# Performance work log

Measured on AMD Instinct MI355X. Metric: run time of the kernel, lower is better.

## Reference

```python
import jax, jax.numpy as jnp
import numpy as np

NUM_EXPERTS = 8
TOP_K = 2
HIDDEN = 1024
INTER = 4096
STD = 0.02


def setup_inputs() -> dict:
    key = jax.random.key(0)
    k0, k1, k2, k3 = jax.random.split(key, 4)
    hidden_states = jax.random.normal(k0, (2, 2048, HIDDEN), dtype=jnp.float32)
    gate_w = jax.random.normal(k1, (NUM_EXPERTS, HIDDEN), dtype=jnp.float32) * (HIDDEN ** -0.5)
    w1 = jax.random.normal(k2, (NUM_EXPERTS, INTER, HIDDEN), dtype=jnp.float32) * STD  # c_fc.weight
    w2 = jax.random.normal(k3, (NUM_EXPERTS, HIDDEN, INTER), dtype=jnp.float32) * STD  # c_proj.weight
    return {"hidden_states": hidden_states, "gate_w": gate_w, "w1": w1, "w2": w2}


def reference(hidden_states, gate_w, w1, w2):
    B, S, H = hidden_states.shape
    x = hidden_states.reshape(-1, H)                      # [T, H]
    T = x.shape[0]
    # ---- routing ----
    router_logits = x @ gate_w.T                          # [T, E]
    top_vals, top_idx = jax.lax.top_k(router_logits, TOP_K)
    router_weights = jax.nn.softmax(top_vals.astype(jnp.float32), axis=-1).astype(x.dtype)
    # dense combine matrix with exactly top_k nonzeros per row (math-equivalent
    # to the sort/grouped-GEMM/scatter-combine pipeline in the torch module)
    combine = jnp.zeros((T, NUM_EXPERTS), x.dtype).at[
        jnp.arange(T)[:, None], top_idx
    ].set(router_weights)                                 # [T, E]
    # ---- experts ----
    h = jax.nn.gelu(jnp.einsum('th,eih->eti', x, w1), approximate=False)  # [E, T, I]
    y = jnp.einsum('eti,ehi->eth', h, w2)                 # [E, T, H]
    out = jnp.einsum('eth,te->th', y, combine)            # weighted combine
    return out.reshape(B, S, H), router_logits
```

## Files before the change

### kernel.cpp

```cpp
#include <hip/hip_runtime.h>

#define T 4096
#define Hdim 1024
#define Idim 4096
#define NE 8
#define OUT0 4194304
#define SPLITK 2
#define BK 64

#define SLOT_CAP 9216

#define W1B_OFF 0u
#define W2B_OFF 67108864u
#define XB_OFF  134217728u
#define HB_OFF  142606336u
#define YB_OFF  218103808u
#define META_OFF 255852544u
#define M_COUNTS 0
#define M_CURS   8
#define M_OFFS   16
#define M_TEXP   32
#define M_TSLOT  8224
#define M_STOK   16416
#define M_TWF    25632

typedef short bf16x8 __attribute__((ext_vector_type(8)));
typedef float f32x4  __attribute__((ext_vector_type(4)));

__device__ __forceinline__ unsigned short f2bf(float f) {
    unsigned int b = __float_as_uint(f);
    b += 0x7fffu + ((b >> 16) & 1u);
    return (unsigned short)(b >> 16);
}
__device__ __forceinline__ float bf2f(unsigned short s) {
    return __uint_as_float(((unsigned int)s) << 16);
}

__device__ __forceinline__ void gl_lds16(const void* g, void* l) {
    __builtin_amdgcn_global_load_lds((const __attribute__((address_space(1))) void*)g,
                                     (__attribute__((address_space(3))) void*)l,
                                     16, 0, 0);
}

__global__ void zero_k(int* meta) {
    int i = blockIdx.x * blockDim.x + threadIdx.x;
    if (i < 16) meta[i] = 0;
    if (i < SLOT_CAP) meta[M_STOK + i] = -1;
}

__global__ void cvt_w_k(const float* __restrict__ w1, const float* __restrict__ w2,
                        unsigned short* __restrict__ w1b, unsigned short* __restrict__ w2b,
                        int n4each) {
    int i = blockIdx.x * blockDim.x + threadIdx.x;
    const float4* src; ushort4* dst; int j;
    if (i < n4each) { src = (const float4*)w1; dst = (ushort4*)w1b; j = i; }
    else            { src = (const float4*)w2; dst = (ushort4*)w2b; j = i - n4each; }
    float4 v = src[j];
    ushort4 o;
    o.x = f2bf(v.x); o.y = f2bf(v.y); o.z = f2bf(v.z); o.w = f2bf(v.w);
    dst[j] = o;
}

__global__ void router_k(const float* __restrict__ x, const float* __restrict__ gw,
                         float* __restrict__ logits_out, int* __restrict__ texp,
                         float* __restrict__ twf, int* __restrict__ counts,
                         unsigned short* __restrict__ xb) {
    int wv = threadIdx.x >> 6, lane = threadIdx.x & 63;
    int t = blockIdx.x * 4 + wv;
    const float* xp = x + (size_t)t * Hdim;
    unsigned short* xbp = xb + (size_t)t * Hdim;
    float s[NE];
    #pragma unroll
    for (int e = 0; e < NE; e++) s[e] = 0.f;
    #pragma unroll
    for (int j = 0; j < 16; j++) {
        float xv = xp[lane + 64 * j];
        xbp[lane + 64 * j] = f2bf(xv);
        #pragma unroll
        for (int e = 0; e < NE; e++) s[e] += xv * gw[e * Hdim + lane + 64 * j];
    }
    #pragma unroll
    for (int e = 0; e < NE; e++) {
        #pragma unroll
        for (int off = 32; off > 0; off >>= 1) s[e] += __shfl_xor(s[e], off);
    }
    if (lane == 0) {
        #pragma unroll
        for (int e = 0; e < NE; e++) logits_out[t * NE + e] = s[e];
        int i0 = 0; float v0 = s[0];
        #pragma unroll
        for (int e = 1; e < NE; e++) if (s[e] > v0) { v0 = s[e]; i0 = e; }
        int i1 = -1; float v1 = -3.4e38f;
        #pragma unroll
        for (int e = 0; e < NE; e++) if (e != i0 && s[e] > v1) { v1 = s[e]; i1 = e; }
        float e1 = expf(v1 - v0);
        float inv = 1.f / (1.f + e1);
        texp[2 * t] = i0; texp[2 * t + 1] = i1;
        twf[2 * t] = inv; twf[2 * t + 1] = e1 * inv;
        atomicAdd(&counts[i0], 1);
        atomicAdd(&counts[i1], 1);
    }
}

__global__ void offsets_k(const int* __restrict__ counts, int* __restrict__ offs) {
    if (threadIdx.x == 0 && blockIdx.x == 0) {
        int a = 0; offs[0] = 0;
        for (int e = 0; e < NE; e++) { a += (counts[e] + 127) & ~127; offs[e + 1] = a; }
    }
}

__global__ void assign_k(const int* __restrict__ texp, const int* __restrict__ offs,
                         int* __restrict__ curs, int* __restrict__ stok, int* __restrict__ tslot) {
    int p = blockIdx.x * blockDim.x + threadIdx.x;
    int e = texp[p];
    int slot = offs[e] + atomicAdd(&curs[e], 1);
    stok[slot] = p >> 1;
    tslot[p] = slot;
}

__global__ __launch_bounds__(256) void gemm1_k(
    const unsigned short* __restrict__ xb, const unsigned short* __restrict__ w1b,
    const int* __restrict__ offs, const int* __restrict__ stok,
    unsigned short* __restrict__ hb) {
    __shared__ __align__(16) unsigned short As[128 * BK];
    __shared__ __align__(16) unsigned short Bs[128 * BK];
    const int rt = blockIdx.y, ct = blockIdx.x;
    const int row0 = rt * 128;
    if (row0 >= offs[NE]) return;
    int e = 0;
    #pragma unroll
    for (int q = 1; q < NE; q++) if (offs[q] <= row0) e = q;

    const int tid = threadIdx.x;
    const int lane = tid & 63, wv = tid >> 6;
    const int srow = lane >> 3;
    const int schunk = (lane & 7) ^ srow;

    const unsigned short* gA[4]; const unsigned short* gB[4];
    unsigned short *lA[4], *lB[4];
    #pragma unroll
    for (int i = 0; i < 4; i++) {
        int r = wv * 32 + i * 8 + srow;
        int t = stok[row0 + r]; if (t < 0) t = 0;
        gA[i] = xb + (size_t)t * Hdim + schunk * 8;
        gB[i] = w1b + ((size_t)e * Idim + ct * 128 + r) * Hdim + schunk * 8;
        lA[i] = As + (wv * 32 + i * 8) * BK;
        lB[i] = Bs + (wv * 32 + i * 8) * BK;
    }

    f32x4 acc[4][4] = {};
    const int mrow = (wv & 1) * 64, ncol = (wv >> 1) * 64;
    const int fr = lane & 15, qd = lane >> 4;

    for (int kk = 0; kk < Hdim; kk += BK) {
        #pragma unroll
        for (int i = 0; i < 4; i++) {
            gl_lds16(gA[i] + kk, lA[i]);
            gl_lds16(gB[i] + kk, lB[i]);
        }
        __syncthreads();
        #pragma unroll
        for (int ko = 0; ko < 2; ko++) {
            bf16x8 af[4], bff[4];
            #pragma unroll
            for (int mi = 0; mi < 4; mi++)
                af[mi]  = *(const bf16x8*)&As[(mrow + mi * 16 + fr) * BK + ((((ko << 2) | qd) ^ (fr & 7)) << 3)];
            #pragma unroll
            for (int ni = 0; ni < 4; ni++)
                bff[ni] = *(const bf16x8*)&Bs[(ncol + ni * 16 + fr) * BK + ((((ko << 2) | qd) ^ (fr & 7)) << 3)];
            #pragma unroll
            for (int mi = 0; mi < 4; mi++)
                #pragma unroll
                for (int ni = 0; ni < 4; ni++)
                    acc[mi][ni] = __builtin_amdgcn_mfma_f32_16x16x32_bf16(af[mi], bff[ni], acc[mi][ni], 0, 0, 0);
        }
        __syncthreads();
    }
    #pragma unroll
    for (int mi = 0; mi < 4; mi++) {
        #pragma unroll
        for (int ni = 0; ni < 4; ni++) {
            #pragma unroll
            for (int r = 0; r < 4; r++) {
                int row = row0 + mrow + mi * 16 + qd * 4 + r;
                int col = ct * 128 + ncol + ni * 16 + fr;
                float v = acc[mi][ni][r];
                float u = v * (1.f + 0.044715f * v * v);
                float g = v / (1.f + __expf(-1.5957691216f * u));
                hb[(size_t)row * Idim + col] = f2bf(g);
            }
        }
    }
}

__global__ __launch_bounds__(256) void gemm2_k(
    const unsigned short* __restrict__ hb, const unsigned short* __restrict__ w2b,
    const int* __restrict__ offs, unsigned short* __restrict__ y16) {
    __shared__ __align__(16) unsigned short As[128 * BK];
    __shared__ __align__(16) unsigned short Bs[128 * BK];
    const int id = blockIdx.x;
    const int k8 = id & 7;
    const int j  = id >> 3;
    const int ct = j & 7;
    const int j8 = j >> 3;
    const int rtL = j8 % 9, kz = j8 / 9;
    const int rt = k8 * 9 + rtL;
    const int row0 = rt * 128;
    if (row0 >= offs[NE]) return;
    int e = 0;
    #pragma unroll
    for (int q = 1; q < NE; q++) if (offs[q] <= row0) e = q;

    const int tid = threadIdx.x;
    const int lane = tid & 63, wv = tid >> 6;
    const int srow = lane >> 3;
    const int schunk = (lane & 7) ^ srow;

    const unsigned short* gA[4]; const unsigned short* gB[4];
    unsigned short *lA[4], *lB[4];
    #pragma unroll
    for (int i = 0; i < 4; i++) {
        int r = wv * 32 + i * 8 + srow;
        gA[i] = hb + (size_t)(row0 + r) * Idim + schunk * 8;
        gB[i] = w2b + ((size_t)e * Hdim + ct * 128 + r) * Idim + schunk * 8;
        lA[i] = As + (wv * 32 + i * 8) * BK;
        lB[i] = Bs + (wv * 32 + i * 8) * BK;
    }

    f32x4 acc[4][4] = {};
    const int mrow = (wv & 1) * 64, ncol = (wv >> 1) * 64;
    const int fr = lane & 15, qd = lane >> 4;

    const int k0 = kz * (Idim / SPLITK), k1 = k0 + (Idim / SPLITK);
    for (int kk = k0; kk < k1; kk += BK) {
        #pragma unroll
        for (int i = 0; i < 4; i++) {
            gl_lds16(gA[i] + kk, lA[i]);
            gl_lds16(gB[i] + kk, lB[i]);
        }
        __syncthreads();
        #pragma unroll
        for (int ko = 0; ko < 2; ko++) {
            bf16x8 af[4], bff[4];
            #pragma unroll
            for (int mi = 0; mi < 4; mi++)
                af[mi]  = *(const bf16x8*)&As[(mrow + mi * 16 + fr) * BK + ((((ko << 2) | qd) ^ (fr & 7)) << 3)];
            #pragma unroll
            for (int ni = 0; ni < 4; ni++)
                bff[ni] = *(const bf16x8*)&Bs[(ncol + ni * 16 + fr) * BK + ((((ko << 2) | qd) ^ (fr & 7)) << 3)];
            #pragma unroll
            for (int mi = 0; mi < 4; mi++)
                #pragma unroll
                for (int ni = 0; ni < 4; ni++)
                    acc[mi][ni] = __builtin_amdgcn_mfma_f32_16x16x32_bf16(af[mi], bff[ni], acc[mi][ni], 0, 0, 0);
        }
        __syncthreads();
    }
    unsigned short* yk = y16 + (size_t)kz * SLOT_CAP * Hdim;
    #pragma unroll
    for (int mi = 0; mi < 4; mi++) {
        #pragma unroll
        for (int ni = 0; ni < 4; ni++) {
            #pragma unroll
            for (int r = 0; r < 4; r++) {
                int row = row0 + mrow + mi * 16 + qd * 4 + r;
                int col = ct * 128 + ncol + ni * 16 + fr;
                yk[(size_t)row * Hdim + col] = f2bf(acc[mi][ni][r]);
            }
        }
    }
}

__global__ void combine_k(const unsigned short* __restrict__ y16, const int* __restrict__ tslot,
                          const float* __restrict__ twf, float* __restrict__ out) {
    int i = blockIdx.x * blockDim.x + threadIdx.x;
    int t = i >> 7, rem = i & 127;
    int s0 = tslot[2 * t], s1 = tslot[2 * t + 1];
    float w0 = twf[2 * t], w1 = twf[2 * t + 1];
    const uint4* y0 = (const uint4*)(y16);
    const uint4* y1 = (const uint4*)(y16 + (size_t)SLOT_CAP * Hdim);
    uint4 a0 = y0[(size_t)s0 * 128 + rem];
    uint4 a1 = y1[(size_t)s0 * 128 + rem];
    uint4 b0 = y0[(size_t)s1 * 128 + rem];
    uint4 b1 = y1[(size_t)s1 * 128 + rem];
    float o[8];
    #pragma unroll
    for (int j = 0; j < 4; j++) {
        unsigned int ua0 = ((const unsigned int*)&a0)[j], ua1 = ((const unsigned int*)&a1)[j];
        unsigned int ub0 = ((const unsigned int*)&b0)[j], ub1 = ((const unsigned int*)&b1)[j];
        float alo = bf2f((unsigned short)ua0) + bf2f((unsigned short)ua1);
        float ahi = bf2f((unsigned short)(ua0 >> 16)) + bf2f((unsigned short)(ua1 >> 16));
        float blo = bf2f((unsigned short)ub0) + bf2f((unsigned short)ub1);
        float bhi = bf2f((unsigned short)(ub0 >> 16)) + bf2f((unsigned short)(ub1 >> 16));
        o[2 * j]     = w0 * alo + w1 * blo;
        o[2 * j + 1] = w0 * ahi + w1 * bhi;
    }
    float4* out4 = (float4*)out;
    out4[2 * i]     = make_float4(o[0], o[1], o[2], o[3]);
    out4[2 * i + 1] = make_float4(o[4], o[5], o[6], o[7]);
}

extern "C" void kernel_launch(void* const* d_in, const int* in_sizes, int n_in,
                              void* d_out, int out_size, void* d_ws, size_t ws_size,
                              hipStream_t stream) {
    const float* x  = (const float*)d_in[0];
    const float* gw = (const float*)d_in[1];
    const float* w1 = (const float*)d_in[2];
    const float* w2 = (const float*)d_in[3];
    float* out = (float*)d_out;

    char* ws = (char*)d_ws;
    unsigned short* w1b = (unsigned short*)(ws + W1B_OFF);
    unsigned short* w2b = (unsigned short*)(ws + W2B_OFF);
    unsigned short* xb  = (unsigned short*)(ws + XB_OFF);
    unsigned short* hb  = (unsigned short*)(ws + HB_OFF);
    unsigned short* y16 = (unsigned short*)(ws + YB_OFF);
    int*            meta = (int*)(ws + META_OFF);
    int* counts = meta + M_COUNTS;
    int* curs   = meta + M_CURS;
    int* offs   = meta + M_OFFS;
    int* texp   = meta + M_TEXP;
    int* tslot  = meta + M_TSLOT;
    int* stok   = meta + M_STOK;
    float* twf  = (float*)(meta + M_TWF);

    zero_k<<<36, 256, 0, stream>>>(meta);
    cvt_w_k<<<65536, 256, 0, stream>>>(w1, w2, w1b, w2b, NE * Idim * Hdim / 4);
    router_k<<<T / 4, 256, 0, stream>>>(x, gw, out + OUT0, texp, twf, counts, xb);
    offsets_k<<<1, 64, 0, stream>>>(counts, offs);
    assign_k<<<32, 256, 0, stream>>>(texp, offs, curs, stok, tslot);
    gemm1_k<<<dim3(Idim / 128, SLOT_CAP / 128), 256, 0, stream>>>(xb, w1b, offs, stok, hb);
    gemm2_k<<<(Hdim / 128) * (SLOT_CAP / 128) * SPLITK, 256, 0, stream>>>(hb, w2b, offs, y16);
    combine_k<<<T * Hdim / 8 / 256, 256, 0, stream>>>(y16, tslot, twf, out);
}
```

Baseline: 672.3 us.

## Register-prefetch next K tile in expert GEMMs instead of direct global-to-LDS loads

Replaces the direct global_load_lds async copies in both expert GEMM kernels with register-staged prefetch. The next K-slice is loaded into registers while MFMAs run on the current LDS tile, then written to LDS between two barriers. This aims to hide global load latency behind compute, which the previous load-then-sync loop could not do. The cost is extra VGPRs, which may lower occupancy, plus an additional barrier per iteration.

```diff
diff --git a/kernel.cpp b/kernel.cpp
--- a/kernel.cpp
+++ b/kernel.cpp
@@ -36,12 +36,6 @@
     return __uint_as_float(((unsigned int)s) << 16);
 }
 
-__device__ __forceinline__ void gl_lds16(const void* g, void* l) {
-    __builtin_amdgcn_global_load_lds((const __attribute__((address_space(1))) void*)g,
-                                     (__attribute__((address_space(3))) void*)l,
-                                     16, 0, 0);
-}
-
 __global__ void zero_k(int* meta) {
     int i = blockIdx.x * blockDim.x + threadIdx.x;
     if (i < 16) meta[i] = 0;
@@ -137,28 +131,38 @@
     const int schunk = (lane & 7) ^ srow;
 
     const unsigned short* gA[4]; const unsigned short* gB[4];
-    unsigned short *lA[4], *lB[4];
+    unsigned short *lds_a[4], *lds_b[4];
     #pragma unroll
     for (int i = 0; i < 4; i++) {
         int r = wv * 32 + i * 8 + srow;
         int t = stok[row0 + r]; if (t < 0) t = 0;
         gA[i] = xb + (size_t)t * Hdim + schunk * 8;
         gB[i] = w1b + ((size_t)e * Idim + ct * 128 + r) * Hdim + schunk * 8;
-        lA[i] = As + (wv * 32 + i * 8) * BK;
-        lB[i] = Bs + (wv * 32 + i * 8) * BK;
+        lds_a[i] = As + (wv * 32 + i * 8) * BK + lane * 8;
+        lds_b[i] = Bs + (wv * 32 + i * 8) * BK + lane * 8;
     }
 
     f32x4 acc[4][4] = {};
     const int mrow = (wv & 1) * 64, ncol = (wv >> 1) * 64;
     const int fr = lane & 15, qd = lane >> 4;
 
-    for (int kk = 0; kk < Hdim; kk += BK) {
-        #pragma unroll
-        for (int i = 0; i < 4; i++) {
-            gl_lds16(gA[i] + kk, lA[i]);
-            gl_lds16(gB[i] + kk, lB[i]);
-        }
-        __syncthreads();
+    uint4 ra[4], rb[4];
+    #pragma unroll
+    for (int i = 0; i < 4; i++) { ra[i] = *(const uint4*)(gA[i]); rb[i] = *(const uint4*)(gB[i]); }
+    #pragma unroll
+    for (int i = 0; i < 4; i++) { *(uint4*)lds_a[i] = ra[i]; *(uint4*)lds_b[i] = rb[i]; }
+    __syncthreads();
+
+    const int NIT = Hdim / BK;
+    for (int it = 0; it < NIT; it++) {
+        if (it + 1 < NIT) {
+            const int nk = (it + 1) * BK;
+            #pragma unroll
+            for (int i = 0; i < 4; i++) {
+                ra[i] = *(const uint4*)(gA[i] + nk);
+                rb[i] = *(const uint4*)(gB[i] + nk);
+            }
+        }
         #pragma unroll
         for (int ko = 0; ko < 2; ko++) {
             bf16x8 af[4], bff[4];
@@ -174,7 +178,12 @@
                 for (int ni = 0; ni < 4; ni++)
                     acc[mi][ni] = __builtin_amdgcn_mfma_f32_16x16x32_bf16(af[mi], bff[ni], acc[mi][ni], 0, 0, 0);
         }
-        __syncthreads();
+        if (it + 1 < NIT) {
+            __syncthreads();
+            #pragma unroll
+            for (int i = 0; i < 4; i++) { *(uint4*)lds_a[i] = ra[i]; *(uint4*)lds_b[i] = rb[i]; }
+            __syncthreads();
+        }
     }
     #pragma unroll
     for (int mi = 0; mi < 4; mi++) {
@@ -217,28 +226,38 @@
     const int schunk = (lane & 7) ^ srow;
 
     const unsigned short* gA[4]; const unsigned short* gB[4];
-    unsigned short *lA[4], *lB[4];
+    unsigned short *lds_a[4], *lds_b[4];
     #pragma unroll
     for (int i = 0; i < 4; i++) {
         int r = wv * 32 + i * 8 + srow;
         gA[i] = hb + (size_t)(row0 + r) * Idim + schunk * 8;
         gB[i] = w2b + ((size_t)e * Hdim + ct * 128 + r) * Idim + schunk * 8;
-        lA[i] = As + (wv * 32 + i * 8) * BK;
-        lB[i] = Bs + (wv * 32 + i * 8) * BK;
+        lds_a[i] = As + (wv * 32 + i * 8) * BK + lane * 8;
+        lds_b[i] = Bs + (wv * 32 + i * 8) * BK + lane * 8;
     }
 
     f32x4 acc[4][4] = {};
     const int mrow = (wv & 1) * 64, ncol = (wv >> 1) * 64;
     const int fr = lane & 15, qd = lane >> 4;
 
-    const int k0 = kz * (Idim / SPLITK), k1 = k0 + (Idim / SPLITK);
-    for (int kk = k0; kk < k1; kk += BK) {
-        #pragma unroll
-        for (int i = 0; i < 4; i++) {
-            gl_lds16(gA[i] + kk, lA[i]);
-            gl_lds16(gB[i] + kk, lB[i]);
-        }
-        __syncthreads();
+    const int k0 = kz * (Idim / SPLITK);
+    uint4 ra[4], rb[4];
+    #pragma unroll
+    for (int i = 0; i < 4; i++) { ra[i] = *(const uint4*)(gA[i] + k0); rb[i] = *(const uint4*)(gB[i] + k0); }
+    #pragma unroll
+    for (int i = 0; i < 4; i++) { *(uint4*)lds_a[i] = ra[i]; *(uint4*)lds_b[i] = rb[i]; }
+    __syncthreads();
+
+    const int NIT = (Idim / SPLITK) / BK;
+    for (int it = 0; it < NIT; it++) {
+        if (it + 1 < NIT) {
+            const int nk = k0 + (it + 1) * BK;
+            #pragma unroll
+            for (int i = 0; i < 4; i++) {
+                ra[i] = *(const uint4*)(gA[i] + nk);
+                rb[i] = *(const uint4*)(gB[i] + nk);
+            }
+        }
         #pragma unroll
         for (int ko = 0; ko < 2; ko++) {
             bf16x8 af[4], bff[4];
@@ -254,7 +273,12 @@
                 for (int ni = 0; ni < 4; ni++)
                     acc[mi][ni] = __builtin_amdgcn_mfma_f32_16x16x32_bf16(af[mi], bff[ni], acc[mi][ni], 0, 0, 0);
         }
-        __syncthreads();
+        if (it + 1 < NIT) {
+            __syncthreads();
+            #pragma unroll
+            for (int i = 0; i < 4; i++) { *(uint4*)lds_a[i] = ra[i]; *(uint4*)lds_b[i] = rb[i]; }
+            __syncthreads();
+        }
     }
     unsigned short* yk = y16 + (size_t)kz * SLOT_CAP * Hdim;
     #pragma unroll
```

Result: slower. 1.248 ms (+85.7%).

## Register-prefetch next K tile in expert GEMMs instead of direct global-to-LDS loads

Applied to the files above, without the earlier changes.

Both expert GEMM kernels drop the global_load_lds direct-to-LDS path. They now load the next K tile into registers while the MFMA loop runs on the current LDS tile, then store it to LDS between two barriers. The goal is to overlap global-memory latency with compute, where the old loop issued loads and waited at a barrier before any math. Launch bounds now request 2 blocks per CU. The cost is extra VGPRs for the prefetch buffers, an additional barrier per iteration, and explicit LDS writes.

```diff
diff --git a/kernel.cpp b/kernel.cpp
--- a/kernel.cpp
+++ b/kernel.cpp
@@ -36,12 +36,6 @@
     return __uint_as_float(((unsigned int)s) << 16);
 }
 
-__device__ __forceinline__ void gl_lds16(const void* g, void* l) {
-    __builtin_amdgcn_global_load_lds((const __attribute__((address_space(1))) void*)g,
-                                     (__attribute__((address_space(3))) void*)l,
-                                     16, 0, 0);
-}
-
 __global__ void zero_k(int* meta) {
     int i = blockIdx.x * blockDim.x + threadIdx.x;
     if (i < 16) meta[i] = 0;
@@ -118,7 +112,16 @@
     tslot[p] = slot;
 }
 
-__global__ __launch_bounds__(256) void gemm1_k(
+#define PF_LOAD(base_off) \
+    pa0 = *(const uint4*)(gA0 + (base_off)); pa1 = *(const uint4*)(gA1 + (base_off)); \
+    pa2 = *(const uint4*)(gA2 + (base_off)); pa3 = *(const uint4*)(gA3 + (base_off)); \
+    pb0 = *(const uint4*)(gB0 + (base_off)); pb1 = *(const uint4*)(gB1 + (base_off)); \
+    pb2 = *(const uint4*)(gB2 + (base_off)); pb3 = *(const uint4*)(gB3 + (base_off));
+#define PF_STORE() \
+    *(uint4*)la0 = pa0; *(uint4*)la1 = pa1; *(uint4*)la2 = pa2; *(uint4*)la3 = pa3; \
+    *(uint4*)lb0 = pb0; *(uint4*)lb1 = pb1; *(uint4*)lb2 = pb2; *(uint4*)lb3 = pb3;
+
+__global__ __launch_bounds__(256, 2) void gemm1_k(
     const unsigned short* __restrict__ xb, const unsigned short* __restrict__ w1b,
     const int* __restrict__ offs, const int* __restrict__ stok,
     unsigned short* __restrict__ hb) {
@@ -136,29 +139,41 @@
     const int srow = lane >> 3;
     const int schunk = (lane & 7) ^ srow;
 
-    const unsigned short* gA[4]; const unsigned short* gB[4];
-    unsigned short *lA[4], *lB[4];
-    #pragma unroll
-    for (int i = 0; i < 4; i++) {
-        int r = wv * 32 + i * 8 + srow;
-        int t = stok[row0 + r]; if (t < 0) t = 0;
-        gA[i] = xb + (size_t)t * Hdim + schunk * 8;
-        gB[i] = w1b + ((size_t)e * Idim + ct * 128 + r) * Hdim + schunk * 8;
-        lA[i] = As + (wv * 32 + i * 8) * BK;
-        lB[i] = Bs + (wv * 32 + i * 8) * BK;
-    }
+    int r0 = wv * 32 + 0 * 8 + srow, r1 = wv * 32 + 1 * 8 + srow;
+    int r2 = wv * 32 + 2 * 8 + srow, r3 = wv * 32 + 3 * 8 + srow;
+    int t0 = stok[row0 + r0]; if (t0 < 0) t0 = 0;
+    int t1 = stok[row0 + r1]; if (t1 < 0) t1 = 0;
+    int t2 = stok[row0 + r2]; if (t2 < 0) t2 = 0;
+    int t3 = stok[row0 + r3]; if (t3 < 0) t3 = 0;
+    const unsigned short* gA0 = xb + (size_t)t0 * Hdim + schunk * 8;
+    const unsigned short* gA1 = xb + (size_t)t1 * Hdim + schunk * 8;
+    const unsigned short* gA2 = xb + (size_t)t2 * Hdim + schunk * 8;
+    const unsigned short* gA3 = xb + (size_t)t3 * Hdim + schunk * 8;
+    const unsigned short* gB0 = w1b + ((size_t)e * Idim + ct * 128 + r0) * Hdim + schunk * 8;
+    const unsigned short* gB1 = w1b + ((size_t)e * Idim + ct * 128 + r1) * Hdim + schunk * 8;
+    const unsigned short* gB2 = w1b + ((size_t)e * Idim + ct * 128 + r2) * Hdim + schunk * 8;
+    const unsigned short* gB3 = w1b + ((size_t)e * Idim + ct * 128 + r3) * Hdim + schunk * 8;
+    unsigned short* la0 = As + (wv * 32 + 0 * 8) * BK + lane * 8;
+    unsigned short* la1 = As + (wv * 32 + 1 * 8) * BK + lane * 8;
+    unsigned short* la2 = As + (wv * 32 + 2 * 8) * BK + lane * 8;
+    unsigned short* la3 = As + (wv * 32 + 3 * 8) * BK + lane * 8;
+    unsigned short* lb0 = Bs + (wv * 32 + 0 * 8) * BK + lane * 8;
+    unsigned short* lb1 = Bs + (wv * 32 + 1 * 8) * BK + lane * 8;
+    unsigned short* lb2 = Bs + (wv * 32 + 2 * 8) * BK + lane * 8;
+    unsigned short* lb3 = Bs + (wv * 32 + 3 * 8) * BK + lane * 8;
 
     f32x4 acc[4][4] = {};
     const int mrow = (wv & 1) * 64, ncol = (wv >> 1) * 64;
     const int fr = lane & 15, qd = lane >> 4;
 
-    for (int kk = 0; kk < Hdim; kk += BK) {
-        #pragma unroll
-        for (int i = 0; i < 4; i++) {
-            gl_lds16(gA[i] + kk, lA[i]);
-            gl_lds16(gB[i] + kk, lB[i]);
-        }
-        __syncthreads();
+    uint4 pa0, pa1, pa2, pa3, pb0, pb1, pb2, pb3;
+    PF_LOAD(0)
+    PF_STORE()
+    __syncthreads();
+
+    const int NIT = Hdim / BK;
+    for (int it = 0; it < NIT; it++) {
+        if (it + 1 < NIT) { PF_LOAD((it + 1) * BK) }
         #pragma unroll
         for (int ko = 0; ko < 2; ko++) {
             bf16x8 af[4], bff[4];
@@ -174,7 +189,11 @@
                 for (int ni = 0; ni < 4; ni++)
                     acc[mi][ni] = __builtin_amdgcn_mfma_f32_16x16x32_bf16(af[mi], bff[ni], acc[mi][ni], 0, 0, 0);
         }
-        __syncthreads();
+        if (it + 1 < NIT) {
+            __syncthreads();
+            PF_STORE()
+            __syncthreads();
+        }
     }
     #pragma unroll
     for (int mi = 0; mi < 4; mi++) {
@@ -193,7 +212,7 @@
     }
 }
 
-__global__ __launch_bounds__(256) void gemm2_k(
+__global__ __launch_bounds__(256, 2) void gemm2_k(
     const unsigned short* __restrict__ hb, const unsigned short* __restrict__ w2b,
     const int* __restrict__ offs, unsigned short* __restrict__ y16) {
     __shared__ __align__(16) unsigned short As[128 * BK];
@@ -216,29 +235,38 @@
     const int srow = lane >> 3;
     const int schunk = (lane & 7) ^ srow;
 
-    const unsigned short* gA[4]; const unsigned short* gB[4];
-    unsigned short *lA[4], *lB[4];
-    #pragma unroll
-    for (int i = 0; i < 4; i++) {
-        int r = wv * 32 + i * 8 + srow;
-        gA[i] = hb + (size_t)(row0 + r) * Idim + schunk * 8;
-        gB[i] = w2b + ((size_t)e * Hdim + ct * 128 + r) * Idim + schunk * 8;
-        lA[i] = As + (wv * 32 + i * 8) * BK;
-        lB[i] = Bs + (wv * 32 + i * 8) * BK;
-    }
+    int r0 = wv * 32 + 0 * 8 + srow, r1 = wv * 32 + 1 * 8 + srow;
+    int r2 = wv * 32 + 2 * 8 + srow, r3 = wv * 32 + 3 * 8 + srow;
+    const unsigned short* gA0 = hb + (size_t)(row0 + r0) * Idim + schunk * 8;
+    const unsigned short* gA1 = hb + (size_t)(row0 + r1) * Idim + schunk * 8;
+    const unsigned short* gA2 = hb + (size_t)(row0 + r2) * Idim + schunk * 8;
+    const unsigned short* gA3 = hb + (size_t)(row0 + r3) * Idim + schunk * 8;
+    const unsigned short* gB0 = w2b + ((size_t)e * Hdim + ct * 128 + r0) * Idim + schunk * 8;
+    const unsigned short* gB1 = w2b + ((size_t)e * Hdim + ct * 128 + r1) * Idim + schunk * 8;
+    const unsigned short* gB2 = w2b + ((size_t)e * Hdim + ct * 128 + r2) * Idim + schunk * 8;
+    const unsigned short* gB3 = w2b + ((size_t)e * Hdim + ct * 128 + r3) * Idim + schunk * 8;
+    unsigned short* la0 = As + (wv * 32 + 0 * 8) * BK + lane * 8;
+    unsigned short* la1 = As + (wv * 32 + 1 * 8) * BK + lane * 8;
+    unsigned short* la2 = As + (wv * 32 + 2 * 8) * BK + lane * 8;
+    unsigned short* la3 = As + (wv * 32 + 3 * 8) * BK + lane * 8;
+    unsigned short* lb0 = Bs + (wv * 32 + 0 * 8) * BK + lane * 8;
+    unsigned short* lb1 = Bs + (wv * 32 + 1 * 8) * BK + lane * 8;
+    unsigned short* lb2 = Bs + (wv * 32 + 2 * 8) * BK + lane * 8;
+    unsigned short* lb3 = Bs + (wv * 32 + 3 * 8) * BK + lane * 8;
 
     f32x4 acc[4][4] = {};
     const int mrow = (wv & 1) * 64, ncol = (wv >> 1) * 64;
     const int fr = lane & 15, qd = lane >> 4;
 
-    const int k0 = kz * (Idim / SPLITK), k1 = k0 + (Idim / SPLITK);
-    for (int kk = k0; kk < k1; kk += BK) {
-        #pragma unroll
-        for (int i = 0; i < 4; i++) {
-            gl_lds16(gA[i] + kk, lA[i]);
-            gl_lds16(gB[i] + kk, lB[i]);
-        }
-        __syncthreads();
+    const int k0 = kz * (Idim / SPLITK);
+    uint4 pa0, pa1, pa2, pa3, pb0, pb1, pb2, pb3;
+    PF_LOAD(k0)
+    PF_STORE()
+    __syncthreads();
+
+    const int NIT = (Idim / SPLITK) / BK;
+    for (int it = 0; it < NIT; it++) {
+        if (it + 1 < NIT) { PF_LOAD(k0 + (it + 1) * BK) }
         #pragma unroll
         for (int ko = 0; ko < 2; ko++) {
             bf16x8 af[4], bff[4];
@@ -254,7 +282,11 @@
                 for (int ni = 0; ni < 4; ni++)
                     acc[mi][ni] = __builtin_amdgcn_mfma_f32_16x16x32_bf16(af[mi], bff[ni], acc[mi][ni], 0, 0, 0);
         }
-        __syncthreads();
+        if (it + 1 < NIT) {
+            __syncthreads();
+            PF_STORE()
+            __syncthreads();
+        }
     }
     unsigned short* yk = y16 + (size_t)kz * SLOT_CAP * Hdim;
     #pragma unroll
```

Result: faster. 631.6 us (-6.1%).
